# Kernel tuning notes

Measured on AMD Instinct MI355X. Metric: run time of the kernel, lower is better.

## Reference

```python
import jax, jax.numpy as jnp
import numpy as np
import math

SCALES = (3, 5)
NUM_CLASSES = 10
D_NEIGHBOR = 64
NUM_GROUPS = 8  # min(8, d_neighbor)
GN_EPS = 1e-5


def setup_inputs() -> dict:
    key = jax.random.key(0)
    k0, k1, k2 = jax.random.split(key, 3)
    B, C, H, W = 8, NUM_CLASSES, 384, 384
    in_ch = 4 * len(SCALES)  # 8
    x = jax.random.normal(k0, (B, C, H, W), jnp.float32)
    W1 = jax.random.normal(k1, (D_NEIGHBOR, in_ch), jnp.float32) / np.sqrt(in_ch).astype(np.float32)
    b1 = jnp.zeros((D_NEIGHBOR,), jnp.float32)
    gn_w = jnp.ones((D_NEIGHBOR,), jnp.float32)
    gn_b = jnp.zeros((D_NEIGHBOR,), jnp.float32)
    W2 = jax.random.normal(k2, (D_NEIGHBOR, D_NEIGHBOR), jnp.float32) / np.sqrt(D_NEIGHBOR).astype(np.float32)
    b2 = jnp.zeros((D_NEIGHBOR,), jnp.float32)
    return {"x": x, "W1": W1, "b1": b1, "gn_w": gn_w, "gn_b": gn_b, "W2": W2, "b2": b2}


def _box_sum(P, k):
    """Depthwise k x k box-filter sum with replicate ('edge') padding."""
    pad = k // 2
    C = P.shape[1]
    Pp = jnp.pad(P, ((0, 0), (0, 0), (pad, pad), (pad, pad)), mode="edge")
    kern = jnp.ones((C, 1, k, k), P.dtype)
    return jax.lax.conv_general_dilated(
        Pp, kern, window_strides=(1, 1), padding="VALID",
        feature_group_count=C, dimension_numbers=("NCHW", "OIHW", "NCHW"))


def _neighbor_features(P):
    # P: (B, C, H, W) soft probabilities
    C = P.shape[1]
    log_C = math.log(NUM_CLASSES)
    feats = []
    for k in SCALES:
        K = float(k * k)
        S = _box_sum(P, k)                       # (B, C, H, W) window sums
        match = (P * (S - P)).sum(axis=1, keepdims=True) / (K - 1.0)
        maj = S.max(axis=1, keepdims=True) / K
        Pbar = S / K
        Pc = jnp.maximum(Pbar, 1e-8)
        ent = -(Pc * jnp.log(Pc)).sum(axis=1, keepdims=True)
        uni = 1.0 - ent / log_C
        S2 = _box_sum(P * P, k)
        var = (S2 / K - Pbar * Pbar).sum(axis=1, keepdims=True)
        feats += [match, maj, uni, var]
    return jnp.concatenate(feats, axis=1)        # (B, 4*len(SCALES), H, W)


def _group_norm(h, gn_w, gn_b):
    B, D, H, W = h.shape
    hg = h.reshape(B, NUM_GROUPS, D // NUM_GROUPS, H, W)
    mu = hg.mean(axis=(2, 3, 4), keepdims=True)
    var = hg.var(axis=(2, 3, 4), keepdims=True)
    hn = ((hg - mu) * jax.lax.rsqrt(var + GN_EPS)).reshape(B, D, H, W)
    return hn * gn_w[None, :, None, None] + gn_b[None, :, None, None]


def reference(x, W1, b1, gn_w, gn_b, W2, b2):
    P = jax.nn.softmax(x, axis=1)                       # (B, C, H, W)
    f = _neighbor_features(P)                           # (B, 8, H, W)
    h = jnp.einsum("bchw,dc->bdhw", f, W1) + b1[None, :, None, None]  # 1x1 conv
    h = _group_norm(h, gn_w, gn_b)
    h = jax.nn.gelu(h, approximate=False)               # torch default GELU (erf)
    out = jnp.einsum("bchw,dc->bdhw", h, W2) + b2[None, :, None, None]
    return out
```

## Files before the change

kernel.cpp:

```cpp
#include <hip/hip_runtime.h>
#include <math.h>

#define Bn 8
#define Cn 10
#define Hd 384
#define Wd 384
#define HW (Hd*Wd)
#define TX 32
#define TY 8
#define TLX 36
#define TLY 12
#define TSZ (TLX*TLY)
#define BLOCKS_PER_IMG 576
#define TILES_X 12

typedef __attribute__((ext_vector_type(8))) short s8v;
typedef __attribute__((ext_vector_type(4))) float f4v;

__device__ __forceinline__ unsigned short f2bf(float f) {
    unsigned u = __builtin_bit_cast(unsigned, f);
    u += 0x7fffu + ((u >> 16) & 1u);
    return (unsigned short)(u >> 16);
}

__device__ __forceinline__ float gelu_erf(float h) {
    float z  = 0.70710678118654752f * h;
    float az = fabsf(z);
    float t  = __builtin_amdgcn_rcpf(1.0f + 0.3275911f * az);
    float poly = ((((1.061405429f * t - 1.453152027f) * t + 1.421413741f) * t
                   - 0.284496736f) * t + 0.254829592f) * t;
    float e = __expf(-az * az);
    float erf_z = copysignf(1.0f - poly * e, z);
    return 0.5f * h * (1.0f + erf_z);
}

__global__ __launch_bounds__(256) void kA(const float* __restrict__ x,
                                          float* __restrict__ fout) {
    __shared__ float4 Pt4[TSZ * 3];
    const int bid = blockIdx.x;
    const int b   = bid / BLOCKS_PER_IMG;
    const int t   = bid % BLOCKS_PER_IMG;
    const int ty  = t / TILES_X, tx = t % TILES_X;
    const int x0  = tx * TX, y0 = ty * TY;
    const int tid = threadIdx.x;
    const float* xb = x + (size_t)b * Cn * HW;

    for (int i = tid; i < TSZ; i += 256) {
        int ly = i / TLX, lx = i % TLX;
        int gy = y0 + ly - 2; gy = max(0, min(Hd - 1, gy));
        int gx = x0 + lx - 2; gx = max(0, min(Wd - 1, gx));
        const float* px = xb + gy * Wd + gx;
        float v[Cn];
        float m = -1e30f;
        #pragma unroll
        for (int c = 0; c < Cn; c++) { v[c] = px[c * HW]; m = fmaxf(m, v[c]); }
        float s = 0.f;
        #pragma unroll
        for (int c = 0; c < Cn; c++) { v[c] = __expf(v[c] - m); s += v[c]; }
        float inv = 1.0f / s;
        float U = 0.f;
        #pragma unroll
        for (int c = 0; c < Cn; c++) { v[c] *= inv; U += v[c] * v[c]; }
        Pt4[i * 3 + 0] = make_float4(v[0], v[1], v[2], v[3]);
        Pt4[i * 3 + 1] = make_float4(v[4], v[5], v[6], v[7]);
        Pt4[i * 3 + 2] = make_float4(v[8], v[9], U, 0.f);
    }
    __syncthreads();

    const int lx = tid % TX, ly = tid / TX;
    const float4* base = &Pt4[((ly + 2) * TLX + (lx + 2)) * 3];

    float S5[Cn], S3[Cn], pc[Cn];
    float U5 = 0.f, U3 = 0.f, Uc = 0.f;
    #pragma unroll
    for (int c = 0; c < Cn; c++) { S5[c] = 0.f; S3[c] = 0.f; }

    #pragma unroll
    for (int dy = -2; dy <= 2; dy++) {
        #pragma unroll
        for (int dx = -2; dx <= 2; dx++) {
            const float4* rp = base + (dy * TLX + dx) * 3;
            float4 r0 = rp[0], r1 = rp[1], r2 = rp[2];
            float vv[Cn] = {r0.x, r0.y, r0.z, r0.w, r1.x, r1.y, r1.z, r1.w,
                            r2.x, r2.y};
            const bool inner = (dy >= -1 && dy <= 1 && dx >= -1 && dx <= 1);
            #pragma unroll
            for (int c = 0; c < Cn; c++) {
                S5[c] += vv[c];
                if (inner) S3[c] += vv[c];
            }
            U5 += r2.z;
            if (inner) U3 += r2.z;
            if (dy == 0 && dx == 0) {
                #pragma unroll
                for (int c = 0; c < Cn; c++) pc[c] = vv[c];
                Uc = r2.z;
            }
        }
    }

    float dot3 = 0.f, dot5 = 0.f, maj3 = -1e30f, maj5 = -1e30f;
    float ent3 = 0.f, ent5 = 0.f, sq3 = 0.f, sq5 = 0.f;
    #pragma unroll
    for (int c = 0; c < Cn; c++) {
        dot3 += pc[c] * S3[c];
        dot5 += pc[c] * S5[c];
        maj3 = fmaxf(maj3, S3[c]);
        maj5 = fmaxf(maj5, S5[c]);
        float q3 = fmaxf(S3[c] * (1.f / 9.f), 1e-8f);  ent3 -= q3 * __logf(q3);
        float q5 = fmaxf(S5[c] * (1.f / 25.f), 1e-8f); ent5 -= q5 * __logf(q5);
        float pb3 = S3[c] * (1.f / 9.f);  sq3 += pb3 * pb3;
        float pb5 = S5[c] * (1.f / 25.f); sq5 += pb5 * pb5;
    }

    const float invlogC = 1.0f / 2.302585092994046f;
    float f0 = (dot3 - Uc) * (1.f / 8.f);
    float f1 = maj3 * (1.f / 9.f);
    float f2 = 1.f - ent3 * invlogC;
    float f3 = U3 * (1.f / 9.f) - sq3;
    float f4 = (dot5 - Uc) * (1.f / 24.f);
    float f5 = maj5 * (1.f / 25.f);
    float f6 = 1.f - ent5 * invlogC;
    float f7 = U5 * (1.f / 25.f) - sq5;

    int p = b * HW + (y0 + ly) * Wd + (x0 + lx);
    float4* o = (float4*)(fout + (size_t)p * 8);
    o[0] = make_float4(f0, f1, f2, f3);
    o[1] = make_float4(f4, f5, f6, f7);
}

__global__ __launch_bounds__(256) void kA2(const float* __restrict__ f,
                                           double* __restrict__ stats) {
    const int blk = blockIdx.x;
    const int b = blk / 72, sub = blk % 72;
    const int base = b * HW + sub * 2048;
    const int tid = threadIdx.x;

    float s[8];
    float q[36];
    #pragma unroll
    for (int i = 0; i < 8; i++) s[i] = 0.f;
    #pragma unroll
    for (int i = 0; i < 36; i++) q[i] = 0.f;

    for (int j = 0; j < 8; j++) {
        int p = base + j * 256 + tid;
        const float4* fv = (const float4*)(f + (size_t)p * 8);
        float4 a = fv[0], c4 = fv[1];
        float fl[8] = {a.x, a.y, a.z, a.w, c4.x, c4.y, c4.z, c4.w};
        int idx = 0;
        #pragma unroll
        for (int c = 0; c < 8; c++) {
            s[c] += fl[c];
            #pragma unroll
            for (int cp = c; cp < 8; cp++) { q[idx] += fl[c] * fl[cp]; idx++; }
        }
    }

    #pragma unroll
    for (int c = 0; c < 8; c++)
        for (int o = 32; o >= 1; o >>= 1) s[c] += __shfl_xor(s[c], o);
    #pragma unroll
    for (int i = 0; i < 36; i++)
        for (int o = 32; o >= 1; o >>= 1) q[i] += __shfl_xor(q[i], o);

    __shared__ float red[4][44];
    int lane = tid & 63, wv = tid >> 6;
    if (lane == 0) {
        #pragma unroll
        for (int c = 0; c < 8; c++) red[wv][c] = s[c];
        #pragma unroll
        for (int i = 0; i < 36; i++) red[wv][8 + i] = q[i];
    }
    __syncthreads();
    if (tid < 44) {
        float tot = red[0][tid] + red[1][tid] + red[2][tid] + red[3][tid];
        atomicAdd(&stats[b * 44 + tid], (double)tot);
    }
}

__global__ __launch_bounds__(512) void kB(const double* __restrict__ stats,
                                          const float* __restrict__ W1,
                                          const float* __restrict__ b1,
                                          const float* __restrict__ gnw,
                                          const float* __restrict__ gnb,
                                          float* __restrict__ ga,
                                          float* __restrict__ gb) {
    const int tid = threadIdx.x;
    const int b = tid >> 6, d = tid & 63;
    const double* st = stats + b * 44;
    const double invN = 1.0 / (double)HW;

    double m[8];
    #pragma unroll
    for (int c = 0; c < 8; c++) m[c] = st[c] * invN;
    double w[8];
    #pragma unroll
    for (int c = 0; c < 8; c++) w[c] = (double)W1[d * 8 + c];

    double wv = 0.0;
    #pragma unroll
    for (int c = 0; c < 8; c++) wv += w[c] * m[c];

    double quad = 0.0;
    int idx = 8;
    #pragma unroll
    for (int c = 0; c < 8; c++) {
        #pragma unroll
        for (int cp = c; cp < 8; cp++) {
            double e2 = st[idx] * invN; idx++;
            quad += (c == cp ? 1.0 : 2.0) * w[c] * w[cp] * e2;
        }
    }
    double bb  = (double)b1[d];
    double mu  = wv + bb;
    double eh2 = quad + 2.0 * bb * wv + bb * bb;

    double gm = mu, gq = eh2;
    #pragma unroll
    for (int o = 1; o < 8; o <<= 1) { gm += __shfl_xor(gm, o); gq += __shfl_xor(gq, o); }
    gm *= 0.125; gq *= 0.125;
    double var = gq - gm * gm;
    double rs  = rsqrt(var + 1e-5);

    float A  = (float)rs * gnw[d];
    float Bs = gnb[d] - (float)(gm * rs) * gnw[d];
    ga[tid] = A;
    gb[tid] = Bs;
}

__global__ __launch_bounds__(256) void kC2(const float* __restrict__ f,
                                           const float* __restrict__ W1,
                                           const float* __restrict__ b1,
                                           const float* __restrict__ W2,
                                           const float* __restrict__ b2,
                                           const float* __restrict__ ga,
                                           const float* __restrict__ gb,
                                           float* __restrict__ out) {
    __shared__ unsigned gl[256 * 33];
    const int b    = blockIdx.x / BLOCKS_PER_IMG;
    const int tile = blockIdx.x % BLOCKS_PER_IMG;
    const int pix0 = tile * 256;
    const int tid  = threadIdx.x;

    {
        const float4* fv = (const float4*)(f + ((size_t)(b * HW + pix0 + tid)) * 8);
        float4 A = fv[0], Bv = fv[1];
        float fl[8] = {A.x, A.y, A.z, A.w, Bv.x, Bv.y, Bv.z, Bv.w};
        const float* gaB = ga + b * 64;
        const float* gbB = gb + b * 64;
        unsigned* row = &gl[tid * 33];
        #pragma unroll
        for (int d2 = 0; d2 < 32; d2++) {
            float h0 = b1[2 * d2], h1 = b1[2 * d2 + 1];
            #pragma unroll
            for (int c = 0; c < 8; c++) {
                h0 += W1[(2 * d2) * 8 + c] * fl[c];
                h1 += W1[(2 * d2 + 1) * 8 + c] * fl[c];
            }
            h0 = h0 * gaB[2 * d2]     + gbB[2 * d2];
            h1 = h1 * gaB[2 * d2 + 1] + gbB[2 * d2 + 1];
            float g0 = gelu_erf(h0), g1 = gelu_erf(h1);
            unsigned pk;
            asm("v_cvt_pk_bf16_f32 %0, %1, %2" : "=v"(pk) : "v"(g0), "v"(g1));
            row[d2] = pk;
        }
    }
    __syncthreads();

    const int w    = tid >> 6;
    const int lane = tid & 63;
    const int quad = lane >> 4;
    const int col  = lane & 15;

    s8v wfr[4][2];
    #pragma unroll
    for (int u = 0; u < 4; u++) {
        const float* wr = W2 + (size_t)(16 * u + col) * 64 + quad * 8;
        #pragma unroll
        for (int kc = 0; kc < 2; kc++) {
            const float4* w4 = (const float4*)(wr + 32 * kc);
            float4 x0 = w4[0], x1 = w4[1];
            union { unsigned short us[8]; s8v v; } cv;
            cv.us[0] = f2bf(x0.x); cv.us[1] = f2bf(x0.y);
            cv.us[2] = f2bf(x0.z); cv.us[3] = f2bf(x0.w);
            cv.us[4] = f2bf(x1.x); cv.us[5] = f2bf(x1.y);
            cv.us[6] = f2bf(x1.z); cv.us[7] = f2bf(x1.w);
            wfr[u][kc] = cv.v;
        }
    }

    f4v acc2[4][4];
    #pragma unroll
    for (int u = 0; u < 4; u++) {
        float bv = b2[16 * u + col];
        #pragma unroll
        for (int t = 0; t < 4; t++) {
            f4v a0; a0[0] = bv; a0[1] = bv; a0[2] = bv; a0[3] = bv;
            acc2[t][u] = a0;
        }
    }

    #pragma unroll
    for (int kc = 0; kc < 2; kc++) {
        s8v gfr[4];
        #pragma unroll
        for (int t = 0; t < 4; t++) {
            int px = 64 * w + 16 * t + col;
            const unsigned* r = &gl[px * 33 + kc * 16 + quad * 4];
            union { unsigned u4[4]; s8v v; } cv;
            cv.u4[0] = r[0]; cv.u4[1] = r[1]; cv.u4[2] = r[2]; cv.u4[3] = r[3];
            gfr[t] = cv.v;
        }
        #pragma unroll
        for (int u = 0; u < 4; u++)
            #pragma unroll
            for (int t = 0; t < 4; t++)
                acc2[t][u] = __builtin_amdgcn_mfma_f32_16x16x32_bf16(
                    gfr[t], wfr[u][kc], acc2[t][u], 0, 0, 0);
    }

    float* ob = out + (size_t)b * 64 * HW + pix0;
    #pragma unroll
    for (int u = 0; u < 4; u++) {
        float* oe = ob + (size_t)(16 * u + col) * HW + 64 * w + quad * 4;
        #pragma unroll
        for (int t = 0; t < 4; t++) {
            float4 sv = make_float4(acc2[t][u][0], acc2[t][u][1],
                                    acc2[t][u][2], acc2[t][u][3]);
            *(float4*)(oe + 16 * t) = sv;
        }
    }
}

extern "C" void kernel_launch(void* const* d_in, const int* in_sizes, int n_in,
                              void* d_out, int out_size, void* d_ws, size_t ws_size,
                              hipStream_t stream) {
    const float* x   = (const float*)d_in[0];
    const float* W1  = (const float*)d_in[1];
    const float* b1  = (const float*)d_in[2];
    const float* gnw = (const float*)d_in[3];
    const float* gnb = (const float*)d_in[4];
    const float* W2  = (const float*)d_in[5];
    const float* b2  = (const float*)d_in[6];
    float* out = (float*)d_out;

    char* ws = (char*)d_ws;
    const size_t FBYTES = (size_t)Bn * HW * 8 * sizeof(float);
    float*  fbuf  = (float*)ws;
    double* stats = (double*)(ws + FBYTES);
    float*  ga    = (float*)(ws + FBYTES + 8 * 44 * sizeof(double));
    float*  gbuf  = ga + Bn * 64;

    hipMemsetAsync(stats, 0, 8 * 44 * sizeof(double), stream);
    kA<<<Bn * BLOCKS_PER_IMG, 256, 0, stream>>>(x, fbuf);
    kA2<<<576, 256, 0, stream>>>(fbuf, stats);
    kB<<<1, 512, 0, stream>>>(stats, W1, b1, gnw, gnb, ga, gbuf);
    kC2<<<Bn * BLOCKS_PER_IMG, 256, 0, stream>>>(fbuf, W1, b1, W2, b2, ga, gbuf, out);
}
```

Before: 446.3 us.

## Fuse group-norm statistics into feature kernel and fold finalize into output kernel

The feature kernel now accumulates the per-image sums and second moments of the 8 features directly (wave shuffles, shared reduction, double atomics), which removes the separate stats pass that re-read the feature buffer. The group-norm scale/shift finalize moves into the output kernel, where 64 threads per block recompute it into shared memory; this drops two launches but repeats that small computation in every block. The 5x5 window loop is also restructured to sum row by row with the outer loop kept rolled, which may reduce code size and register pressure. The cost is 4608 blocks each issuing 44 double atomics onto the same 352 addresses, which risks contention.

```diff
diff --git a/kernel.cpp b/kernel.cpp
--- a/kernel.cpp
+++ b/kernel.cpp
@@ -35,8 +35,10 @@
 }
 
 __global__ __launch_bounds__(256) void kA(const float* __restrict__ x,
-                                          float* __restrict__ fout) {
+                                          float* __restrict__ fout,
+                                          double* __restrict__ stats) {
     __shared__ float4 Pt4[TSZ * 3];
+    __shared__ float red[4][44];
     const int bid = blockIdx.x;
     const int b   = bid / BLOCKS_PER_IMG;
     const int t   = bid % BLOCKS_PER_IMG;
@@ -70,33 +72,50 @@
     const int lx = tid % TX, ly = tid / TX;
     const float4* base = &Pt4[((ly + 2) * TLX + (lx + 2)) * 3];
 
-    float S5[Cn], S3[Cn], pc[Cn];
-    float U5 = 0.f, U3 = 0.f, Uc = 0.f;
+    float S5[Cn], S3[Cn];
+    float U5 = 0.f, U3 = 0.f;
     #pragma unroll
     for (int c = 0; c < Cn; c++) { S5[c] = 0.f; S3[c] = 0.f; }
 
-    #pragma unroll
+    #pragma unroll 1
     for (int dy = -2; dy <= 2; dy++) {
-        #pragma unroll
-        for (int dx = -2; dx <= 2; dx++) {
-            const float4* rp = base + (dy * TLX + dx) * 3;
-            float4 r0 = rp[0], r1 = rp[1], r2 = rp[2];
+        float R5[Cn], R3[Cn];
+        float u5r = 0.f, u3r = 0.f;
+        #pragma unroll
+        for (int c = 0; c < Cn; c++) { R5[c] = 0.f; R3[c] = 0.f; }
+        const float4* rowp = base + (dy * TLX - 2) * 3;
+        #pragma unroll
+        for (int dx = 0; dx < 5; dx++) {
+            float4 r0 = rowp[dx * 3 + 0];
+            float4 r1 = rowp[dx * 3 + 1];
+            float4 r2 = rowp[dx * 3 + 2];
             float vv[Cn] = {r0.x, r0.y, r0.z, r0.w, r1.x, r1.y, r1.z, r1.w,
                             r2.x, r2.y};
-            const bool inner = (dy >= -1 && dy <= 1 && dx >= -1 && dx <= 1);
-            #pragma unroll
-            for (int c = 0; c < Cn; c++) {
-                S5[c] += vv[c];
-                if (inner) S3[c] += vv[c];
+            #pragma unroll
+            for (int c = 0; c < Cn; c++) R5[c] += vv[c];
+            u5r += r2.z;
+            if (dx >= 1 && dx <= 3) {
+                #pragma unroll
+                for (int c = 0; c < Cn; c++) R3[c] += vv[c];
+                u3r += r2.z;
             }
-            U5 += r2.z;
-            if (inner) U3 += r2.z;
-            if (dy == 0 && dx == 0) {
-                #pragma unroll
-                for (int c = 0; c < Cn; c++) pc[c] = vv[c];
-                Uc = r2.z;
-            }
-        }
+        }
+        #pragma unroll
+        for (int c = 0; c < Cn; c++) S5[c] += R5[c];
+        U5 += u5r;
+        if ((unsigned)(dy + 1) <= 2u) {
+            #pragma unroll
+            for (int c = 0; c < Cn; c++) S3[c] += R3[c];
+            U3 += u3r;
+        }
+    }
+
+    float pc[Cn], Uc;
+    {
+        float4 c0 = base[0], c1 = base[1], c2 = base[2];
+        pc[0] = c0.x; pc[1] = c0.y; pc[2] = c0.z; pc[3] = c0.w;
+        pc[4] = c1.x; pc[5] = c1.y; pc[6] = c1.z; pc[7] = c1.w;
+        pc[8] = c2.x; pc[9] = c2.y; Uc = c2.z;
     }
 
     float dot3 = 0.f, dot5 = 0.f, maj3 = -1e30f, maj5 = -1e30f;
@@ -114,63 +133,39 @@
     }
 
     const float invlogC = 1.0f / 2.302585092994046f;
-    float f0 = (dot3 - Uc) * (1.f / 8.f);
-    float f1 = maj3 * (1.f / 9.f);
-    float f2 = 1.f - ent3 * invlogC;
-    float f3 = U3 * (1.f / 9.f) - sq3;
-    float f4 = (dot5 - Uc) * (1.f / 24.f);
-    float f5 = maj5 * (1.f / 25.f);
-    float f6 = 1.f - ent5 * invlogC;
-    float f7 = U5 * (1.f / 25.f) - sq5;
+    float fv8[8];
+    fv8[0] = (dot3 - Uc) * (1.f / 8.f);
+    fv8[1] = maj3 * (1.f / 9.f);
+    fv8[2] = 1.f - ent3 * invlogC;
+    fv8[3] = U3 * (1.f / 9.f) - sq3;
+    fv8[4] = (dot5 - Uc) * (1.f / 24.f);
+    fv8[5] = maj5 * (1.f / 25.f);
+    fv8[6] = 1.f - ent5 * invlogC;
+    fv8[7] = U5 * (1.f / 25.f) - sq5;
 
     int p = b * HW + (y0 + ly) * Wd + (x0 + lx);
     float4* o = (float4*)(fout + (size_t)p * 8);
-    o[0] = make_float4(f0, f1, f2, f3);
-    o[1] = make_float4(f4, f5, f6, f7);
-}
-
-__global__ __launch_bounds__(256) void kA2(const float* __restrict__ f,
-                                           double* __restrict__ stats) {
-    const int blk = blockIdx.x;
-    const int b = blk / 72, sub = blk % 72;
-    const int base = b * HW + sub * 2048;
-    const int tid = threadIdx.x;
-
-    float s[8];
-    float q[36];
-    #pragma unroll
-    for (int i = 0; i < 8; i++) s[i] = 0.f;
-    #pragma unroll
-    for (int i = 0; i < 36; i++) q[i] = 0.f;
-
-    for (int j = 0; j < 8; j++) {
-        int p = base + j * 256 + tid;
-        const float4* fv = (const float4*)(f + (size_t)p * 8);
-        float4 a = fv[0], c4 = fv[1];
-        float fl[8] = {a.x, a.y, a.z, a.w, c4.x, c4.y, c4.z, c4.w};
-        int idx = 0;
-        #pragma unroll
-        for (int c = 0; c < 8; c++) {
-            s[c] += fl[c];
-            #pragma unroll
-            for (int cp = c; cp < 8; cp++) { q[idx] += fl[c] * fl[cp]; idx++; }
-        }
-    }
-
-    #pragma unroll
-    for (int c = 0; c < 8; c++)
-        for (int o = 32; o >= 1; o >>= 1) s[c] += __shfl_xor(s[c], o);
-    #pragma unroll
-    for (int i = 0; i < 36; i++)
-        for (int o = 32; o >= 1; o >>= 1) q[i] += __shfl_xor(q[i], o);
-
-    __shared__ float red[4][44];
+    o[0] = make_float4(fv8[0], fv8[1], fv8[2], fv8[3]);
+    o[1] = make_float4(fv8[4], fv8[5], fv8[6], fv8[7]);
+
+    float mv[44];
+    #pragma unroll
+    for (int c = 0; c < 8; c++) mv[c] = fv8[c];
+    {
+        int idx = 8;
+        #pragma unroll
+        for (int c = 0; c < 8; c++)
+            #pragma unroll
+            for (int cp = c; cp < 8; cp++) { mv[idx] = fv8[c] * fv8[cp]; idx++; }
+    }
+    #pragma unroll
+    for (int i = 0; i < 44; i++)
+        for (int o2 = 32; o2 >= 1; o2 >>= 1) mv[i] += __shfl_xor(mv[i], o2);
+
     int lane = tid & 63, wv = tid >> 6;
     if (lane == 0) {
         #pragma unroll
-        for (int c = 0; c < 8; c++) red[wv][c] = s[c];
-        #pragma unroll
-        for (int i = 0; i < 36; i++) red[wv][8 + i] = q[i];
+        for (int i = 0; i < 44; i++) red[wv][i] = mv[i];
     }
     __syncthreads();
     if (tid < 44) {
@@ -179,76 +174,63 @@
     }
 }
 
-__global__ __launch_bounds__(512) void kB(const double* __restrict__ stats,
+__global__ __launch_bounds__(256) void kC(const float* __restrict__ f,
+                                          const double* __restrict__ stats,
                                           const float* __restrict__ W1,
                                           const float* __restrict__ b1,
                                           const float* __restrict__ gnw,
                                           const float* __restrict__ gnb,
-                                          float* __restrict__ ga,
-                                          float* __restrict__ gb) {
-    const int tid = threadIdx.x;
-    const int b = tid >> 6, d = tid & 63;
-    const double* st = stats + b * 44;
-    const double invN = 1.0 / (double)HW;
-
-    double m[8];
-    #pragma unroll
-    for (int c = 0; c < 8; c++) m[c] = st[c] * invN;
-    double w[8];
-    #pragma unroll
-    for (int c = 0; c < 8; c++) w[c] = (double)W1[d * 8 + c];
-
-    double wv = 0.0;
-    #pragma unroll
-    for (int c = 0; c < 8; c++) wv += w[c] * m[c];
-
-    double quad = 0.0;
-    int idx = 8;
-    #pragma unroll
-    for (int c = 0; c < 8; c++) {
-        #pragma unroll
-        for (int cp = c; cp < 8; cp++) {
-            double e2 = st[idx] * invN; idx++;
-            quad += (c == cp ? 1.0 : 2.0) * w[c] * w[cp] * e2;
-        }
-    }
-    double bb  = (double)b1[d];
-    double mu  = wv + bb;
-    double eh2 = quad + 2.0 * bb * wv + bb * bb;
-
-    double gm = mu, gq = eh2;
-    #pragma unroll
-    for (int o = 1; o < 8; o <<= 1) { gm += __shfl_xor(gm, o); gq += __shfl_xor(gq, o); }
-    gm *= 0.125; gq *= 0.125;
-    double var = gq - gm * gm;
-    double rs  = rsqrt(var + 1e-5);
-
-    float A  = (float)rs * gnw[d];
-    float Bs = gnb[d] - (float)(gm * rs) * gnw[d];
-    ga[tid] = A;
-    gb[tid] = Bs;
-}
-
-__global__ __launch_bounds__(256) void kC2(const float* __restrict__ f,
-                                           const float* __restrict__ W1,
-                                           const float* __restrict__ b1,
-                                           const float* __restrict__ W2,
-                                           const float* __restrict__ b2,
-                                           const float* __restrict__ ga,
-                                           const float* __restrict__ gb,
-                                           float* __restrict__ out) {
+                                          const float* __restrict__ W2,
+                                          const float* __restrict__ b2,
+                                          float* __restrict__ out) {
     __shared__ unsigned gl[256 * 33];
+    __shared__ float gaL[64], gbL[64];
     const int b    = blockIdx.x / BLOCKS_PER_IMG;
     const int tile = blockIdx.x % BLOCKS_PER_IMG;
     const int pix0 = tile * 256;
     const int tid  = threadIdx.x;
 
+    if (tid < 64) {
+        const int d = tid;
+        const double* st = stats + b * 44;
+        const double invN = 1.0 / (double)HW;
+        double w[8];
+        #pragma unroll
+        for (int c = 0; c < 8; c++) w[c] = (double)W1[d * 8 + c];
+        double wv = 0.0;
+        #pragma unroll
+        for (int c = 0; c < 8; c++) wv += w[c] * (st[c] * invN);
+        double quad = 0.0;
+        int idx = 8;
+        #pragma unroll
+        for (int c = 0; c < 8; c++) {
+            #pragma unroll
+            for (int cp = c; cp < 8; cp++) {
+                double e2 = st[idx] * invN; idx++;
+                quad += (c == cp ? 1.0 : 2.0) * w[c] * w[cp] * e2;
+            }
+        }
+        double bb  = (double)b1[d];
+        double mu  = wv + bb;
+        double eh2 = quad + 2.0 * bb * wv + bb * bb;
+        double gm = mu, gq = eh2;
+        #pragma unroll
+        for (int o = 1; o < 8; o <<= 1) {
+            gm += __shfl_xor(gm, o);
+            gq += __shfl_xor(gq, o);
+        }
+        gm *= 0.125; gq *= 0.125;
+        double var = gq - gm * gm;
+        double rs  = rsqrt(var + 1e-5);
+        gaL[d] = (float)rs * gnw[d];
+        gbL[d] = gnb[d] - (float)(gm * rs) * gnw[d];
+    }
+    __syncthreads();
+
     {
         const float4* fv = (const float4*)(f + ((size_t)(b * HW + pix0 + tid)) * 8);
         float4 A = fv[0], Bv = fv[1];
         float fl[8] = {A.x, A.y, A.z, A.w, Bv.x, Bv.y, Bv.z, Bv.w};
-        const float* gaB = ga + b * 64;
-        const float* gbB = gb + b * 64;
         unsigned* row = &gl[tid * 33];
         #pragma unroll
         for (int d2 = 0; d2 < 32; d2++) {
@@ -258,8 +240,8 @@
                 h0 += W1[(2 * d2) * 8 + c] * fl[c];
                 h1 += W1[(2 * d2 + 1) * 8 + c] * fl[c];
             }
-            h0 = h0 * gaB[2 * d2]     + gbB[2 * d2];
-            h1 = h1 * gaB[2 * d2 + 1] + gbB[2 * d2 + 1];
+            h0 = h0 * gaL[2 * d2]     + gbL[2 * d2];
+            h1 = h1 * gaL[2 * d2 + 1] + gbL[2 * d2 + 1];
             float g0 = gelu_erf(h0), g1 = gelu_erf(h1);
             unsigned pk;
             asm("v_cvt_pk_bf16_f32 %0, %1, %2" : "=v"(pk) : "v"(g0), "v"(g1));
@@ -349,12 +331,9 @@
     const size_t FBYTES = (size_t)Bn * HW * 8 * sizeof(float);
     float*  fbuf  = (float*)ws;
     double* stats = (double*)(ws + FBYTES);
-    float*  ga    = (float*)(ws + FBYTES + 8 * 44 * sizeof(double));
-    float*  gbuf  = ga + Bn * 64;
 
     hipMemsetAsync(stats, 0, 8 * 44 * sizeof(double), stream);
-    kA<<<Bn * BLOCKS_PER_IMG, 256, 0, stream>>>(x, fbuf);
-    kA2<<<576, 256, 0, stream>>>(fbuf, stats);
-    kB<<<1, 512, 0, stream>>>(stats, W1, b1, gnw, gnb, ga, gbuf);
-    kC2<<<Bn * BLOCKS_PER_IMG, 256, 0, stream>>>(fbuf, W1, b1, W2, b2, ga, gbuf, out);
-}
+    kA<<<Bn * BLOCKS_PER_IMG, 256, 0, stream>>>(x, fbuf, stats);
+    kC<<<Bn * BLOCKS_PER_IMG, 256, 0, stream>>>(fbuf, stats, W1, b1, gnw, gnb,
+                                                W2, b2, out);
+}
```

Result: slower. 473.2 us (+6.0%).
